# Kernel optimization log

Hardware: AMD Instinct MI355X
Metric: run time of the kernel (lower is better)

Reference implementation:

```python
import jax, jax.numpy as jnp
import numpy as np

H, W = 480, 640
NUM_SEM = 12      # len(stuff_labels)+1
NUM_INS = 16      # number of detected instances
NUM_THING = 9     # len(thing_labels)+1
NUM_ITER = 3
GAMMA_SEM = 3.0
GAMMA_INS = 3.0
ALPHA_SEM = 3.0
BETA_SEM = 0.15
ALPHA_INS = 3.0
BETA_INS = 0.15
R_BIL = 2         # bilateral truncation radius


def _gauss1d(sigma):
    r = int(np.ceil(2.0 * sigma))
    x = np.arange(-r, r + 1, dtype=np.float32)
    k = np.exp(-0.5 * (x / sigma) ** 2)
    k /= k.sum()
    return jnp.asarray(k)


def _sep_blur(q, k):
    # normalized Gaussian spatial filter, separable depthwise conv. q: (C,H,W)
    C = q.shape[0]
    K = k.shape[0]
    p = K // 2
    x = q[None]  # (1,C,H,W)
    kh = jnp.broadcast_to(k.reshape(1, 1, K, 1), (C, 1, K, 1))
    x = jax.lax.conv_general_dilated(x, kh, (1, 1), [(p, p), (0, 0)], feature_group_count=C)
    kw = jnp.broadcast_to(k.reshape(1, 1, 1, K), (C, 1, 1, K))
    x = jax.lax.conv_general_dilated(x, kw, (1, 1), [(0, 0), (p, p)], feature_group_count=C)
    return x[0]


def _bilateral(q, image, alpha, beta, R):
    # truncated-window bilateral (joint spatial/color Gaussian), normalized per pixel
    C, Hh, Ww = q.shape
    Ip = jnp.pad(image, ((0, 0), (R, R), (R, R)), mode='edge')
    qp = jnp.pad(q, ((0, 0), (R, R), (R, R)), mode='edge')
    num = jnp.zeros_like(q)
    den = jnp.zeros((Hh, Ww), q.dtype)
    inv2a2 = 1.0 / (2.0 * alpha * alpha)
    inv2b2 = 1.0 / (2.0 * beta * beta)
    for dy in range(2 * R + 1):
        for dx in range(2 * R + 1):
            Ish = P = Ip[:, dy:dy + Hh, dx:dx + Ww]
            cd = jnp.sum((image - Ish) ** 2, axis=0)          # color distance (H,W)
            sd = float((dy - R) ** 2 + (dx - R) ** 2)          # spatial distance
            w = jnp.exp(-sd * inv2a2 - cd * inv2b2)
            num = num + w[None] * qp[:, dy:dy + Hh, dx:dx + Ww]
            den = den + w
    return num / den[None]


def _compat(q, M):
    # torch.mm(M.t(), q.view(Cin,-1)).view(Cout,H,W)
    return jnp.einsum('io,ihw->ohw', M, q)


def setup_inputs() -> dict:
    key = jax.random.key(0)
    ks = jax.random.split(key, 6)
    return {
        'image': jax.random.uniform(ks[0], (3, H, W), jnp.float32),
        'semantic_logits': jax.random.normal(ks[1], (NUM_SEM, H, W), jnp.float32),
        'instance_logits': jax.random.normal(ks[2], (NUM_INS, H, W), jnp.float32),
        'instance_cls_labels': jax.random.randint(ks[3], (NUM_INS,), 0, NUM_THING),
        'sem_spatial_w': 3.0 * jnp.ones((NUM_SEM,), jnp.float32),
        'sem_bilateral_w': 5.0 * jnp.ones((NUM_SEM,), jnp.float32),
        'sem_compat': jnp.eye(NUM_SEM, dtype=jnp.float32),
        'ins_spatial_w': 3.0 * jnp.ones((NUM_THING,), jnp.float32),
        'ins_bilateral_w': 3.0 * jnp.ones((NUM_THING,), jnp.float32),
        'cross_ins_sem': 0.1 * jax.random.normal(ks[4], (NUM_THING, NUM_SEM), jnp.float32),
        'cross_sem_ins': 0.1 * jax.random.normal(ks[5], (NUM_THING, NUM_SEM), jnp.float32),
    }


def reference(image, semantic_logits, instance_logits, instance_cls_labels,
              sem_spatial_w, sem_bilateral_w, sem_compat,
              ins_spatial_w, ins_bilateral_w, cross_ins_sem, cross_sem_ins):
    k_sem = _gauss1d(GAMMA_SEM)
    k_ins = _gauss1d(GAMMA_INS)
    sem_q = jax.nn.softmax(semantic_logits, axis=0)
    ins_q = jax.nn.softmax(instance_logits, axis=0)
    sw = ins_spatial_w[instance_cls_labels][:, None, None]      # (NI,1,1)
    bw = ins_bilateral_w[instance_cls_labels][:, None, None]
    M_is = cross_ins_sem[instance_cls_labels]                   # (NI, NUM_SEM)
    M_si = cross_sem_ins[instance_cls_labels].T                 # (NUM_SEM, NI)
    for _ in range(NUM_ITER):
        sp_sem = sem_spatial_w[:, None, None] * _sep_blur(sem_q, k_sem)
        bl_sem = sem_bilateral_w[:, None, None] * _bilateral(sem_q, image, ALPHA_SEM, BETA_SEM, R_BIL)
        tmp_sem = semantic_logits + _compat(sp_sem + bl_sem, sem_compat)
        sp_ins = sw * _sep_blur(ins_q, k_ins)
        bl_ins = bw * _bilateral(ins_q, image, ALPHA_INS, BETA_INS, R_BIL)
        tmp_ins = instance_logits + sp_ins + bl_ins
        tmp_sem_new = tmp_sem + _compat(jax.nn.softmax(tmp_ins, axis=0), M_is)
        tmp_ins_new = tmp_ins + _compat(jax.nn.softmax(tmp_sem, axis=0), M_si)
        sem_q = jax.nn.softmax(tmp_sem_new, axis=0)
        ins_q = jax.nn.softmax(tmp_ins_new, axis=0)
    return sem_q, ins_q
```

## Files before the change

kernel.cpp:

```cpp
#include <hip/hip_runtime.h>

#define HH   480
#define WW   640
#define HWP  (HH*WW)
#define NSEM 12
#define NINS 16
#define NCH  28

typedef _Float16 f16_t;

union P32 { f16_t h[32]; int4 v[4]; };
union I4H8 { int4 v; f16_t h[8]; };
union I2H4 { int2 v; f16_t h[4]; };
union H4I2 { f16_t h[4]; int2 v; };

__device__ __forceinline__ void gauss13(float k[13]) {
    float s = 0.f;
#pragma unroll
    for (int j = 0; j < 13; ++j) {
        float xx = (float)(j - 6);
        float v  = __expf(-(xx * xx) * (1.f / 18.f));
        k[j] = v; s += v;
    }
    float inv = 1.f / s;
#pragma unroll
    for (int j = 0; j < 13; ++j) k[j] *= inv;
}

template <int N>
__device__ __forceinline__ void softmaxN(const float* __restrict__ in, float* __restrict__ out) {
    float m = in[0];
#pragma unroll
    for (int i = 1; i < N; ++i) m = fmaxf(m, in[i]);
    float s = 0.f;
#pragma unroll
    for (int i = 0; i < N; ++i) { float e = __expf(in[i] - m); out[i] = e; s += e; }
    float inv = 1.f / s;
#pragma unroll
    for (int i = 0; i < N; ++i) out[i] *= inv;
}

__global__ __launch_bounds__(256) void init_kernel(const float* __restrict__ semL,
                                                   const float* __restrict__ insL,
                                                   int4* __restrict__ qcl4,
                                                   f16_t* __restrict__ qpm,
                                                   f16_t* __restrict__ semLh,
                                                   f16_t* __restrict__ insLh) {
    int p = blockIdx.x * 256 + threadIdx.x;
    float v[NINS], o[NINS];
    P32 pk;
#pragma unroll
    for (int i = 0; i < 32; ++i) pk.h[i] = (f16_t)0.f;
#pragma unroll
    for (int i = 0; i < NSEM; ++i) { v[i] = semL[i * HWP + p]; semLh[i * HWP + p] = (f16_t)v[i]; }
    softmaxN<NSEM>(v, o);
#pragma unroll
    for (int i = 0; i < NSEM; ++i) { f16_t h = (f16_t)o[i]; pk.h[i] = h; qpm[i * HWP + p] = h; }
#pragma unroll
    for (int i = 0; i < NINS; ++i) { v[i] = insL[i * HWP + p]; insLh[i * HWP + p] = (f16_t)v[i]; }
    softmaxN<NINS>(v, o);
#pragma unroll
    for (int i = 0; i < NINS; ++i) { f16_t h = (f16_t)o[i]; pk.h[NSEM + i] = h; qpm[(NSEM + i) * HWP + p] = h; }
#pragma unroll
    for (int j = 0; j < 4; ++j) qcl4[p * 4 + j] = pk.v[j];
}

#define BTW 64
#define BTH 32
#define RAWW 80
#define RAWH 44
__global__ __launch_bounds__(256) void blur_fused_kernel(const f16_t* __restrict__ in,
                                                         f16_t* __restrict__ out) {
    __shared__ float raw[RAWH * RAWW];
    __shared__ float hb[RAWH * BTW];
    const int t  = threadIdx.x;
    const int x0 = blockIdx.x * BTW;
    const int y0 = blockIdx.y * BTH;
    const int c  = blockIdx.z;
    const f16_t* __restrict__ plane = in + (size_t)c * HWP;

    float k[13]; gauss13(k);

    for (int idx = t; idx < RAWH * 10; idx += 256) {
        int row = idx / 10, g = idx - row * 10;
        int gy = y0 - 6 + row;
        int gx8 = x0 - 8 + g * 8;
        float4 lo = {0.f,0.f,0.f,0.f}, hi = {0.f,0.f,0.f,0.f};
        if (gy >= 0 && gy < HH && gx8 >= 0 && gx8 <= WW - 8) {
            I4H8 u; u.v = *(const int4*)&plane[gy * WW + gx8];
            lo.x = (float)u.h[0]; lo.y = (float)u.h[1]; lo.z = (float)u.h[2]; lo.w = (float)u.h[3];
            hi.x = (float)u.h[4]; hi.y = (float)u.h[5]; hi.z = (float)u.h[6]; hi.w = (float)u.h[7];
        }
        *(float4*)&raw[row * RAWW + g * 8]     = lo;
        *(float4*)&raw[row * RAWW + g * 8 + 4] = hi;
    }
    __syncthreads();

    for (int idx = t; idx < RAWH * 16; idx += 256) {
        int row = idx >> 4, xg = idx & 15;
        const float* rp = &raw[row * RAWW + xg * 4];
        float f[20];
#pragma unroll
        for (int q4 = 0; q4 < 5; ++q4) {
            float4 v = *(const float4*)&rp[q4 * 4];
            f[q4*4+0]=v.x; f[q4*4+1]=v.y; f[q4*4+2]=v.z; f[q4*4+3]=v.w;
        }
        float4 o;
        float* op = &o.x;
#pragma unroll
        for (int j = 0; j < 4; ++j) {
            float a = 0.f;
#pragma unroll
            for (int i = 0; i < 13; ++i) a = fmaf(k[i], f[j + 2 + i], a);
            op[j] = a;
        }
        *(float4*)&hb[row * BTW + xg * 4] = o;
    }
    __syncthreads();

    {
        const int xg = t & 15;
        const int yg = t >> 4;
        float4 r[14];
#pragma unroll
        for (int i = 0; i < 14; ++i)
            r[i] = *(const float4*)&hb[(yg * 2 + i) * BTW + xg * 4];
#pragma unroll
        for (int j = 0; j < 2; ++j) {
            float a0 = 0.f, a1 = 0.f, a2 = 0.f, a3 = 0.f;
#pragma unroll
            for (int i = 0; i < 13; ++i) {
                float4 v = r[j + i];
                a0 = fmaf(k[i], v.x, a0); a1 = fmaf(k[i], v.y, a1);
                a2 = fmaf(k[i], v.z, a2); a3 = fmaf(k[i], v.w, a3);
            }
            H4I2 s;
            s.h[0] = (f16_t)a0; s.h[1] = (f16_t)a1; s.h[2] = (f16_t)a2; s.h[3] = (f16_t)a3;
            *(int2*)&out[(size_t)c * HWP + (y0 + yg * 2 + j) * WW + (x0 + xg * 4)] = s.v;
        }
    }
}

#define TTW 32
#define TTH 8
#define TWW (TTW + 4)
#define TWH (TTH + 4)
#define TWN (TWW * TWH)

template <bool LAST>
__global__ __launch_bounds__(256, 5) void tail_kernel(const int4* __restrict__ qcl4,
                                                      const f16_t* __restrict__ sp,
                                                      const float* __restrict__ img,
                                                      const f16_t* __restrict__ semLh,
                                                      const f16_t* __restrict__ insLh,
                                                      const float* __restrict__ sem_sw,
                                                      const float* __restrict__ sem_bw,
                                                      const float* __restrict__ sem_compat,
                                                      const float* __restrict__ ins_sw,
                                                      const float* __restrict__ ins_bw,
                                                      const int*   __restrict__ labels,
                                                      const float* __restrict__ cross_is,
                                                      const float* __restrict__ cross_si,
                                                      int4* __restrict__ qclo4,
                                                      f16_t* __restrict__ qpmo,
                                                      float* __restrict__ dout) {
    __shared__ int4  lqA[TWN * 3];
    __shared__ int2  lqB[TWN];
    __shared__ float limg[3 * TWN];
    __shared__ float sC[NSEM * NSEM];
    __shared__ float sMis[NINS * NSEM];
    __shared__ float sMsi[NINS * NSEM];
    __shared__ float sws[NSEM], sbs[NSEM], swi[NINS], sbi[NINS];

    const int t  = threadIdx.x;
    const int tx = t & 31;
    const int ty = t >> 5;
    const int x0 = blockIdx.x * TTW;
    const int y0 = blockIdx.y * TTH;
    const int p  = (y0 + ty) * WW + (x0 + tx);

    if (t < NSEM * NSEM) sC[t] = sem_compat[t];
    if (t < NINS * NSEM) {
        int i = t / NSEM, o = t - i * NSEM;
        sMis[t] = cross_is[labels[i] * NSEM + o];
        sMsi[t] = cross_si[labels[i] * NSEM + o];
    }
    if (t < NSEM) { sws[t] = sem_sw[t]; sbs[t] = sem_bw[t]; }
    if (t < NINS) { int l = labels[t]; swi[t] = ins_sw[l]; sbi[t] = ins_bw[l]; }

#pragma unroll
    for (int j = 0; j < 6; ++j) {
        int idx = t + j * 256;
        if (idx < TWN * 3) {
            int e = idx / 3, s = idx - e * 3;
            int ly = e / TWW, lx = e - ly * TWW;
            int gy = min(max(y0 - 2 + ly, 0), HH - 1);
            int gx = min(max(x0 - 2 + lx, 0), WW - 1);
            lqA[idx] = qcl4[(gy * WW + gx) * 4 + s];
        }
    }
#pragma unroll
    for (int j = 0; j < 2; ++j) {
        int e = t + j * 256;
        if (e < TWN) {
            int ly = e / TWW, lx = e - ly * TWW;
            int gy = min(max(y0 - 2 + ly, 0), HH - 1);
            int gx = min(max(x0 - 2 + lx, 0), WW - 1);
            lqB[e] = ((const int2*)qcl4)[(gy * WW + gx) * 8 + 6];
        }
    }
    for (int idx = t; idx < 3 * TWN; idx += 256) {
        int cc  = idx / TWN;
        int rem = idx - cc * TWN;
        int ly  = rem / TWW, lx = rem - ly * TWW;
        int gy  = min(max(y0 - 2 + ly, 0), HH - 1);
        int gx  = min(max(x0 - 2 + lx, 0), WW - 1);
        limg[idx] = img[(size_t)cc * HWP + gy * WW + gx];
    }
    __syncthreads();

    float wnr[25];
    {
        const int wc = (ty + 2) * TWW + (tx + 2);
        float i0 = limg[wc], i1 = limg[TWN + wc], i2 = limg[2 * TWN + wc];
        float den = 0.f;
        int d = 0;
#pragma unroll
        for (int dy = 0; dy < 5; ++dy) {
#pragma unroll
            for (int dx = 0; dx < 5; ++dx) {
                int nb = (ty + dy) * TWW + (tx + dx);
                float d0 = limg[nb] - i0;
                float d1 = limg[TWN + nb] - i1;
                float d2 = limg[2 * TWN + nb] - i2;
                float cd = d0 * d0 + d1 * d1 + d2 * d2;
                float sd = (float)((dy - 2) * (dy - 2) + (dx - 2) * (dx - 2));
                float wv = __expf(-sd * (1.f / 18.f) - cd * (1.f / 0.045f));
                wnr[d++] = wv; den += wv;
            }
        }
        float inv = 1.f / den;
#pragma unroll
        for (int j = 0; j < 25; ++j) wnr[j] *= inv;
    }

    float bl[NCH];
#pragma unroll
    for (int c = 0; c < NCH; ++c) bl[c] = 0.f;
#pragma unroll
    for (int dy = 0; dy < 5; ++dy) {
        int rb = (ty + dy) * TWW + tx;
#pragma unroll
        for (int dx = 0; dx < 5; ++dx) {
            float w = wnr[dy * 5 + dx];
            int e = rb + dx;
#pragma unroll
            for (int s = 0; s < 3; ++s) {
                I4H8 u; u.v = lqA[e * 3 + s];
#pragma unroll
                for (int i = 0; i < 8; ++i)
                    bl[s * 8 + i] = fmaf((float)u.h[i], w, bl[s * 8 + i]);
            }
            I2H4 ub; ub.v = lqB[e];
#pragma unroll
            for (int i = 0; i < 4; ++i)
                bl[24 + i] = fmaf((float)ub.h[i], w, bl[24 + i]);
        }
    }

    float comb[NSEM];
#pragma unroll
    for (int i = 0; i < NSEM; ++i)
        comb[i] = sws[i] * (float)sp[i * HWP + p] + sbs[i] * bl[i];
    float ts[NSEM];
#pragma unroll
    for (int o = 0; o < NSEM; ++o) {
        float a = (float)semLh[o * HWP + p];
#pragma unroll
        for (int i = 0; i < NSEM; ++i) a = fmaf(sC[i * NSEM + o], comb[i], a);
        ts[o] = a;
    }
    float ti[NINS];
#pragma unroll
    for (int i = 0; i < NINS; ++i)
        ti[i] = (float)insLh[i * HWP + p] + swi[i] * (float)sp[(NSEM + i) * HWP + p] + sbi[i] * bl[NSEM + i];

    float sIns[NINS], sSem[NSEM];
    softmaxN<NINS>(ti, sIns);
    softmaxN<NSEM>(ts, sSem);

    float nts[NSEM];
#pragma unroll
    for (int o = 0; o < NSEM; ++o) {
        float a = ts[o];
#pragma unroll
        for (int i = 0; i < NINS; ++i) a = fmaf(sMis[i * NSEM + o], sIns[i], a);
        nts[o] = a;
    }
    float nti[NINS];
#pragma unroll
    for (int o = 0; o < NINS; ++o) {
        float a = ti[o];
#pragma unroll
        for (int i = 0; i < NSEM; ++i) a = fmaf(sMsi[o * NSEM + i], sSem[i], a);
        nti[o] = a;
    }

    float oq1[NSEM], oq2[NINS];
    softmaxN<NSEM>(nts, oq1);
    softmaxN<NINS>(nti, oq2);

    if (LAST) {
#pragma unroll
        for (int i = 0; i < NSEM; ++i) dout[i * HWP + p] = oq1[i];
#pragma unroll
        for (int i = 0; i < NINS; ++i) dout[(NSEM + i) * HWP + p] = oq2[i];
    } else {
        P32 pk;
#pragma unroll
        for (int i = 0; i < 32; ++i) pk.h[i] = (f16_t)0.f;
#pragma unroll
        for (int i = 0; i < NSEM; ++i) { f16_t h = (f16_t)oq1[i]; pk.h[i] = h; qpmo[i * HWP + p] = h; }
#pragma unroll
        for (int i = 0; i < NINS; ++i) { f16_t h = (f16_t)oq2[i]; pk.h[NSEM + i] = h; qpmo[(NSEM + i) * HWP + p] = h; }
#pragma unroll
        for (int j = 0; j < 4; ++j) qclo4[p * 4 + j] = pk.v[j];
    }
}

extern "C" void kernel_launch(void* const* d_in, const int* in_sizes, int n_in,
                              void* d_out, int out_size, void* d_ws, size_t ws_size,
                              hipStream_t stream) {
    const float* image      = (const float*)d_in[0];
    const float* semL       = (const float*)d_in[1];
    const float* insL       = (const float*)d_in[2];
    const int*   labels     = (const int*)  d_in[3];
    const float* sem_sw     = (const float*)d_in[4];
    const float* sem_bw     = (const float*)d_in[5];
    const float* sem_compat = (const float*)d_in[6];
    const float* ins_sw     = (const float*)d_in[7];
    const float* ins_bw     = (const float*)d_in[8];
    const float* cross_is   = (const float*)d_in[9];
    const float* cross_si   = (const float*)d_in[10];

    char* ws = (char*)d_ws;
    int4*  qclA  = (int4*)ws;                                   ws += (size_t)HWP * 64;
    int4*  qclB  = (int4*)ws;                                   ws += (size_t)HWP * 64;
    f16_t* qpmA  = (f16_t*)ws;                                  ws += (size_t)NCH * HWP * 2;
    f16_t* qpmB  = (f16_t*)ws;                                  ws += (size_t)NCH * HWP * 2;
    f16_t* sp    = (f16_t*)ws;                                  ws += (size_t)NCH * HWP * 2;
    f16_t* semLh = (f16_t*)ws;                                  ws += (size_t)NSEM * HWP * 2;
    f16_t* insLh = (f16_t*)ws;

    const int PIX_BLOCKS = HWP / 256;
    init_kernel<<<PIX_BLOCKS, 256, 0, stream>>>(semL, insL, qclA, qpmA, semLh, insLh);

    dim3 bgrid(WW / BTW, HH / BTH, NCH);
    dim3 tgrid(WW / TTW, HH / TTH);

    blur_fused_kernel<<<bgrid, 256, 0, stream>>>(qpmA, sp);
    tail_kernel<false><<<tgrid, 256, 0, stream>>>(qclA, sp, image, semLh, insLh,
                                                  sem_sw, sem_bw, sem_compat,
                                                  ins_sw, ins_bw, labels,
                                                  cross_is, cross_si, qclB, qpmB, nullptr);
    blur_fused_kernel<<<bgrid, 256, 0, stream>>>(qpmB, sp);
    tail_kernel<false><<<tgrid, 256, 0, stream>>>(qclB, sp, image, semLh, insLh,
                                                  sem_sw, sem_bw, sem_compat,
                                                  ins_sw, ins_bw, labels,
                                                  cross_is, cross_si, qclA, qpmA, nullptr);
    blur_fused_kernel<<<bgrid, 256, 0, stream>>>(qpmA, sp);
    tail_kernel<true><<<tgrid, 256, 0, stream>>>(qclA, sp, image, semLh, insLh,
                                                 sem_sw, sem_bw, sem_compat,
                                                 ins_sw, ins_bw, labels,
                                                 cross_is, cross_si, nullptr, nullptr, (float*)d_out);
}
```

Baseline: 280.8 us.

## Split blur into channel-last horizontal pass and fuse vertical pass into tail

Replaces the planar per-channel fused blur kernel with a horizontal-only pass over the channel-interleaved q buffer. The vertical 13-tap pass is computed inside the tail kernel by reading the horizontally blurred buffer straight from global memory. Logits move to a channel-interleaved f16 buffer, the planar q copy is dropped, the bilateral weight normalisation is folded into a single division, and tail blocks are swizzled. This removes the planar buffer writes and the separate 2D-tiled blur. In exchange, each tail thread does 13 uncached global row reads per pixel, and lowering the launch bound occupancy target raises register pressure.

Result: slower. 651.4 us (+132.0%).

```diff
diff --git a/kernel.cpp b/kernel.cpp
--- a/kernel.cpp
+++ b/kernel.cpp
@@ -9,10 +9,9 @@
 
 typedef _Float16 f16_t;
 
-union P32 { f16_t h[32]; int4 v[4]; };
+union P32  { f16_t h[32]; int4 v[4]; };
 union I4H8 { int4 v; f16_t h[8]; };
 union I2H4 { int2 v; f16_t h[4]; };
-union H4I2 { f16_t h[4]; int2 v; };
 
 __device__ __forceinline__ void gauss13(float k[13]) {
     float s = 0.f;
@@ -43,102 +42,50 @@
 __global__ __launch_bounds__(256) void init_kernel(const float* __restrict__ semL,
                                                    const float* __restrict__ insL,
                                                    int4* __restrict__ qcl4,
-                                                   f16_t* __restrict__ qpm,
-                                                   f16_t* __restrict__ semLh,
-                                                   f16_t* __restrict__ insLh) {
+                                                   int4* __restrict__ lcl4) {
     int p = blockIdx.x * 256 + threadIdx.x;
     float v[NINS], o[NINS];
-    P32 pk;
-#pragma unroll
-    for (int i = 0; i < 32; ++i) pk.h[i] = (f16_t)0.f;
-#pragma unroll
-    for (int i = 0; i < NSEM; ++i) { v[i] = semL[i * HWP + p]; semLh[i * HWP + p] = (f16_t)v[i]; }
+    P32 pk, lk;
+#pragma unroll
+    for (int i = 0; i < 32; ++i) { pk.h[i] = (f16_t)0.f; lk.h[i] = (f16_t)0.f; }
+#pragma unroll
+    for (int i = 0; i < NSEM; ++i) { v[i] = semL[i * HWP + p]; lk.h[i] = (f16_t)v[i]; }
     softmaxN<NSEM>(v, o);
 #pragma unroll
-    for (int i = 0; i < NSEM; ++i) { f16_t h = (f16_t)o[i]; pk.h[i] = h; qpm[i * HWP + p] = h; }
-#pragma unroll
-    for (int i = 0; i < NINS; ++i) { v[i] = insL[i * HWP + p]; insLh[i * HWP + p] = (f16_t)v[i]; }
+    for (int i = 0; i < NSEM; ++i) pk.h[i] = (f16_t)o[i];
+#pragma unroll
+    for (int i = 0; i < NINS; ++i) { v[i] = insL[i * HWP + p]; lk.h[NSEM + i] = (f16_t)v[i]; }
     softmaxN<NINS>(v, o);
 #pragma unroll
-    for (int i = 0; i < NINS; ++i) { f16_t h = (f16_t)o[i]; pk.h[NSEM + i] = h; qpm[(NSEM + i) * HWP + p] = h; }
-#pragma unroll
-    for (int j = 0; j < 4; ++j) qcl4[p * 4 + j] = pk.v[j];
-}
-
-#define BTW 64
-#define BTH 32
-#define RAWW 80
-#define RAWH 44
-__global__ __launch_bounds__(256) void blur_fused_kernel(const f16_t* __restrict__ in,
-                                                         f16_t* __restrict__ out) {
-    __shared__ float raw[RAWH * RAWW];
-    __shared__ float hb[RAWH * BTW];
-    const int t  = threadIdx.x;
-    const int x0 = blockIdx.x * BTW;
-    const int y0 = blockIdx.y * BTH;
-    const int c  = blockIdx.z;
-    const f16_t* __restrict__ plane = in + (size_t)c * HWP;
-
+    for (int i = 0; i < NINS; ++i) pk.h[NSEM + i] = (f16_t)o[i];
+#pragma unroll
+    for (int j = 0; j < 4; ++j) { qcl4[(size_t)p * 4 + j] = pk.v[j]; lcl4[(size_t)p * 4 + j] = lk.v[j]; }
+}
+
+__global__ __launch_bounds__(256) void hpass_kernel(const int4* __restrict__ qcl4,
+                                                    int4* __restrict__ hq4) {
+    int tid = blockIdx.x * 256 + threadIdx.x;
+    int p = tid >> 2;
+    int s = tid & 3;
+    int y = p / WW;
+    int x = p - y * WW;
     float k[13]; gauss13(k);
-
-    for (int idx = t; idx < RAWH * 10; idx += 256) {
-        int row = idx / 10, g = idx - row * 10;
-        int gy = y0 - 6 + row;
-        int gx8 = x0 - 8 + g * 8;
-        float4 lo = {0.f,0.f,0.f,0.f}, hi = {0.f,0.f,0.f,0.f};
-        if (gy >= 0 && gy < HH && gx8 >= 0 && gx8 <= WW - 8) {
-            I4H8 u; u.v = *(const int4*)&plane[gy * WW + gx8];
-            lo.x = (float)u.h[0]; lo.y = (float)u.h[1]; lo.z = (float)u.h[2]; lo.w = (float)u.h[3];
-            hi.x = (float)u.h[4]; hi.y = (float)u.h[5]; hi.z = (float)u.h[6]; hi.w = (float)u.h[7];
-        }
-        *(float4*)&raw[row * RAWW + g * 8]     = lo;
-        *(float4*)&raw[row * RAWW + g * 8 + 4] = hi;
-    }
-    __syncthreads();
-
-    for (int idx = t; idx < RAWH * 16; idx += 256) {
-        int row = idx >> 4, xg = idx & 15;
-        const float* rp = &raw[row * RAWW + xg * 4];
-        float f[20];
-#pragma unroll
-        for (int q4 = 0; q4 < 5; ++q4) {
-            float4 v = *(const float4*)&rp[q4 * 4];
-            f[q4*4+0]=v.x; f[q4*4+1]=v.y; f[q4*4+2]=v.z; f[q4*4+3]=v.w;
-        }
-        float4 o;
-        float* op = &o.x;
-#pragma unroll
-        for (int j = 0; j < 4; ++j) {
-            float a = 0.f;
-#pragma unroll
-            for (int i = 0; i < 13; ++i) a = fmaf(k[i], f[j + 2 + i], a);
-            op[j] = a;
-        }
-        *(float4*)&hb[row * BTW + xg * 4] = o;
-    }
-    __syncthreads();
-
-    {
-        const int xg = t & 15;
-        const int yg = t >> 4;
-        float4 r[14];
-#pragma unroll
-        for (int i = 0; i < 14; ++i)
-            r[i] = *(const float4*)&hb[(yg * 2 + i) * BTW + xg * 4];
-#pragma unroll
-        for (int j = 0; j < 2; ++j) {
-            float a0 = 0.f, a1 = 0.f, a2 = 0.f, a3 = 0.f;
-#pragma unroll
-            for (int i = 0; i < 13; ++i) {
-                float4 v = r[j + i];
-                a0 = fmaf(k[i], v.x, a0); a1 = fmaf(k[i], v.y, a1);
-                a2 = fmaf(k[i], v.z, a2); a3 = fmaf(k[i], v.w, a3);
-            }
-            H4I2 s;
-            s.h[0] = (f16_t)a0; s.h[1] = (f16_t)a1; s.h[2] = (f16_t)a2; s.h[3] = (f16_t)a3;
-            *(int2*)&out[(size_t)c * HWP + (y0 + yg * 2 + j) * WW + (x0 + xg * 4)] = s.v;
-        }
-    }
+    float a[8];
+#pragma unroll
+    for (int i = 0; i < 8; ++i) a[i] = 0.f;
+#pragma unroll
+    for (int t = 0; t < 13; ++t) {
+        int xt = x + t - 6;
+        if ((unsigned)xt < WW) {
+            I4H8 u; u.v = qcl4[(size_t)(p + t - 6) * 4 + s];
+#pragma unroll
+            for (int i = 0; i < 8; ++i) a[i] = fmaf((float)u.h[i], k[t], a[i]);
+        }
+    }
+    I4H8 r;
+#pragma unroll
+    for (int i = 0; i < 8; ++i) r.h[i] = (f16_t)a[i];
+    hq4[tid] = r.v;
 }
 
 #define TTW 32
@@ -148,11 +95,10 @@
 #define TWN (TWW * TWH)
 
 template <bool LAST>
-__global__ __launch_bounds__(256, 5) void tail_kernel(const int4* __restrict__ qcl4,
-                                                      const f16_t* __restrict__ sp,
+__global__ __launch_bounds__(256, 4) void tail_kernel(const int4* __restrict__ qcl4,
+                                                      const int4* __restrict__ hq4,
                                                       const float* __restrict__ img,
-                                                      const f16_t* __restrict__ semLh,
-                                                      const f16_t* __restrict__ insLh,
+                                                      const int4* __restrict__ lcl4,
                                                       const float* __restrict__ sem_sw,
                                                       const float* __restrict__ sem_bw,
                                                       const float* __restrict__ sem_compat,
@@ -162,7 +108,6 @@
                                                       const float* __restrict__ cross_is,
                                                       const float* __restrict__ cross_si,
                                                       int4* __restrict__ qclo4,
-                                                      f16_t* __restrict__ qpmo,
                                                       float* __restrict__ dout) {
     __shared__ int4  lqA[TWN * 3];
     __shared__ int2  lqB[TWN];
@@ -172,12 +117,16 @@
     __shared__ float sMsi[NINS * NSEM];
     __shared__ float sws[NSEM], sbs[NSEM], swi[NINS], sbi[NINS];
 
-    const int t  = threadIdx.x;
-    const int tx = t & 31;
-    const int ty = t >> 5;
-    const int x0 = blockIdx.x * TTW;
-    const int y0 = blockIdx.y * TTH;
-    const int p  = (y0 + ty) * WW + (x0 + tx);
+    const int t = threadIdx.x;
+    const int lid = (int)blockIdx.x;
+    const int swz = (lid & 7) * 150 + (lid >> 3);
+    const int by  = swz / 20;
+    const int bx  = swz - by * 20;
+    const int tx  = t & 31;
+    const int ty  = t >> 5;
+    const int x0  = bx * TTW;
+    const int y0  = by * TTH;
+    const int p   = (y0 + ty) * WW + (x0 + tx);
 
     if (t < NSEM * NSEM) sC[t] = sem_compat[t];
     if (t < NINS * NSEM) {
@@ -196,7 +145,7 @@
             int ly = e / TWW, lx = e - ly * TWW;
             int gy = min(max(y0 - 2 + ly, 0), HH - 1);
             int gx = min(max(x0 - 2 + lx, 0), WW - 1);
-            lqA[idx] = qcl4[(gy * WW + gx) * 4 + s];
+            lqA[idx] = qcl4[((size_t)gy * WW + gx) * 4 + s];
         }
     }
 #pragma unroll
@@ -206,7 +155,7 @@
             int ly = e / TWW, lx = e - ly * TWW;
             int gy = min(max(y0 - 2 + ly, 0), HH - 1);
             int gx = min(max(x0 - 2 + lx, 0), WW - 1);
-            lqB[e] = ((const int2*)qcl4)[(gy * WW + gx) * 8 + 6];
+            lqB[e] = ((const int2*)qcl4)[((size_t)gy * WW + gx) * 8 + 6];
         }
     }
     for (int idx = t; idx < 3 * TWN; idx += 256) {
@@ -217,73 +166,97 @@
         int gx  = min(max(x0 - 2 + lx, 0), WW - 1);
         limg[idx] = img[(size_t)cc * HWP + gy * WW + gx];
     }
+
+    float kv[13]; gauss13(kv);
+    float vac[NCH];
+#pragma unroll
+    for (int c = 0; c < NCH; ++c) vac[c] = 0.f;
+    {
+        const int xc = x0 + tx;
+        const int yb = y0 + ty - 6;
+#pragma unroll
+        for (int tt = 0; tt < 13; ++tt) {
+            int yt = yb + tt;
+            if ((unsigned)yt < HH) {
+                const int4* rp = &hq4[((size_t)yt * WW + xc) * 4];
+                float w = kv[tt];
+                I4H8 u0, u1, u2; I2H4 u3;
+                u0.v = rp[0]; u1.v = rp[1]; u2.v = rp[2];
+                u3.v = ((const int2*)rp)[6];
+#pragma unroll
+                for (int i = 0; i < 8; ++i) vac[i]      = fmaf((float)u0.h[i], w, vac[i]);
+#pragma unroll
+                for (int i = 0; i < 8; ++i) vac[8 + i]  = fmaf((float)u1.h[i], w, vac[8 + i]);
+#pragma unroll
+                for (int i = 0; i < 8; ++i) vac[16 + i] = fmaf((float)u2.h[i], w, vac[16 + i]);
+#pragma unroll
+                for (int i = 0; i < 4; ++i) vac[24 + i] = fmaf((float)u3.h[i], w, vac[24 + i]);
+            }
+        }
+    }
+    I4H8 l0, l1, l2; I2H4 l3;
+    l0.v = lcl4[(size_t)p * 4 + 0];
+    l1.v = lcl4[(size_t)p * 4 + 1];
+    l2.v = lcl4[(size_t)p * 4 + 2];
+    l3.v = ((const int2*)lcl4)[(size_t)p * 8 + 6];
     __syncthreads();
 
-    float wnr[25];
+    float num[NCH];
+#pragma unroll
+    for (int c = 0; c < NCH; ++c) num[c] = 0.f;
+    float den = 0.f;
     {
         const int wc = (ty + 2) * TWW + (tx + 2);
         float i0 = limg[wc], i1 = limg[TWN + wc], i2 = limg[2 * TWN + wc];
-        float den = 0.f;
-        int d = 0;
 #pragma unroll
         for (int dy = 0; dy < 5; ++dy) {
 #pragma unroll
             for (int dx = 0; dx < 5; ++dx) {
-                int nb = (ty + dy) * TWW + (tx + dx);
-                float d0 = limg[nb] - i0;
-                float d1 = limg[TWN + nb] - i1;
-                float d2 = limg[2 * TWN + nb] - i2;
+                int e = (ty + dy) * TWW + (tx + dx);
+                float d0 = limg[e] - i0;
+                float d1 = limg[TWN + e] - i1;
+                float d2 = limg[2 * TWN + e] - i2;
                 float cd = d0 * d0 + d1 * d1 + d2 * d2;
                 float sd = (float)((dy - 2) * (dy - 2) + (dx - 2) * (dx - 2));
-                float wv = __expf(-sd * (1.f / 18.f) - cd * (1.f / 0.045f));
-                wnr[d++] = wv; den += wv;
+                float w  = __expf(-sd * (1.f / 18.f) - cd * (1.f / 0.045f));
+                den += w;
+                I4H8 a0, a1, a2; I2H4 b;
+                a0.v = lqA[e * 3 + 0]; a1.v = lqA[e * 3 + 1]; a2.v = lqA[e * 3 + 2];
+                b.v  = lqB[e];
+#pragma unroll
+                for (int i = 0; i < 8; ++i) num[i]      = fmaf((float)a0.h[i], w, num[i]);
+#pragma unroll
+                for (int i = 0; i < 8; ++i) num[8 + i]  = fmaf((float)a1.h[i], w, num[8 + i]);
+#pragma unroll
+                for (int i = 0; i < 8; ++i) num[16 + i] = fmaf((float)a2.h[i], w, num[16 + i]);
+#pragma unroll
+                for (int i = 0; i < 4; ++i) num[24 + i] = fmaf((float)b.h[i],  w, num[24 + i]);
             }
         }
-        float inv = 1.f / den;
-#pragma unroll
-        for (int j = 0; j < 25; ++j) wnr[j] *= inv;
-    }
-
-    float bl[NCH];
-#pragma unroll
-    for (int c = 0; c < NCH; ++c) bl[c] = 0.f;
-#pragma unroll
-    for (int dy = 0; dy < 5; ++dy) {
-        int rb = (ty + dy) * TWW + tx;
-#pragma unroll
-        for (int dx = 0; dx < 5; ++dx) {
-            float w = wnr[dy * 5 + dx];
-            int e = rb + dx;
-#pragma unroll
-            for (int s = 0; s < 3; ++s) {
-                I4H8 u; u.v = lqA[e * 3 + s];
-#pragma unroll
-                for (int i = 0; i < 8; ++i)
-                    bl[s * 8 + i] = fmaf((float)u.h[i], w, bl[s * 8 + i]);
-            }
-            I2H4 ub; ub.v = lqB[e];
-#pragma unroll
-            for (int i = 0; i < 4; ++i)
-                bl[24 + i] = fmaf((float)ub.h[i], w, bl[24 + i]);
-        }
-    }
+    }
+    const float inv = 1.f / den;
 
     float comb[NSEM];
 #pragma unroll
     for (int i = 0; i < NSEM; ++i)
-        comb[i] = sws[i] * (float)sp[i * HWP + p] + sbs[i] * bl[i];
+        comb[i] = sws[i] * vac[i] + sbs[i] * (num[i] * inv);
     float ts[NSEM];
 #pragma unroll
     for (int o = 0; o < NSEM; ++o) {
-        float a = (float)semLh[o * HWP + p];
+        float a = (o < 8) ? (float)l0.h[o] : (float)l1.h[o - 8];
 #pragma unroll
         for (int i = 0; i < NSEM; ++i) a = fmaf(sC[i * NSEM + o], comb[i], a);
         ts[o] = a;
     }
     float ti[NINS];
 #pragma unroll
-    for (int i = 0; i < NINS; ++i)
-        ti[i] = (float)insLh[i * HWP + p] + swi[i] * (float)sp[(NSEM + i) * HWP + p] + sbi[i] * bl[NSEM + i];
+    for (int i = 0; i < NINS; ++i) {
+        const int c = NSEM + i;
+        float lg = (c < 16) ? (float)l1.h[c - 8]
+                 : (c < 24) ? (float)l2.h[c - 16]
+                            : (float)l3.h[c - 24];
+        ti[i] = lg + swi[i] * vac[c] + sbi[i] * (num[c] * inv);
+    }
 
     float sIns[NINS], sSem[NSEM];
     softmaxN<NINS>(ti, sIns);
@@ -320,11 +293,11 @@
 #pragma unroll
         for (int i = 0; i < 32; ++i) pk.h[i] = (f16_t)0.f;
 #pragma unroll
-        for (int i = 0; i < NSEM; ++i) { f16_t h = (f16_t)oq1[i]; pk.h[i] = h; qpmo[i * HWP + p] = h; }
-#pragma unroll
-        for (int i = 0; i < NINS; ++i) { f16_t h = (f16_t)oq2[i]; pk.h[NSEM + i] = h; qpmo[(NSEM + i) * HWP + p] = h; }
-#pragma unroll
-        for (int j = 0; j < 4; ++j) qclo4[p * 4 + j] = pk.v[j];
+        for (int i = 0; i < NSEM; ++i) pk.h[i] = (f16_t)oq1[i];
+#pragma unroll
+        for (int i = 0; i < NINS; ++i) pk.h[NSEM + i] = (f16_t)oq2[i];
+#pragma unroll
+        for (int j = 0; j < 4; ++j) qclo4[(size_t)p * 4 + j] = pk.v[j];
     }
 }
 
@@ -344,33 +317,29 @@
     const float* cross_si   = (const float*)d_in[10];
 
     char* ws = (char*)d_ws;
-    int4*  qclA  = (int4*)ws;                                   ws += (size_t)HWP * 64;
-    int4*  qclB  = (int4*)ws;                                   ws += (size_t)HWP * 64;
-    f16_t* qpmA  = (f16_t*)ws;                                  ws += (size_t)NCH * HWP * 2;
-    f16_t* qpmB  = (f16_t*)ws;                                  ws += (size_t)NCH * HWP * 2;
-    f16_t* sp    = (f16_t*)ws;                                  ws += (size_t)NCH * HWP * 2;
-    f16_t* semLh = (f16_t*)ws;                                  ws += (size_t)NSEM * HWP * 2;
-    f16_t* insLh = (f16_t*)ws;
+    int4* qclA = (int4*)ws;   ws += (size_t)HWP * 64;
+    int4* qclB = (int4*)ws;   ws += (size_t)HWP * 64;
+    int4* hq   = (int4*)ws;   ws += (size_t)HWP * 64;
+    int4* lcl  = (int4*)ws;
 
     const int PIX_BLOCKS = HWP / 256;
-    init_kernel<<<PIX_BLOCKS, 256, 0, stream>>>(semL, insL, qclA, qpmA, semLh, insLh);
-
-    dim3 bgrid(WW / BTW, HH / BTH, NCH);
-    dim3 tgrid(WW / TTW, HH / TTH);
-
-    blur_fused_kernel<<<bgrid, 256, 0, stream>>>(qpmA, sp);
-    tail_kernel<false><<<tgrid, 256, 0, stream>>>(qclA, sp, image, semLh, insLh,
-                                                  sem_sw, sem_bw, sem_compat,
-                                                  ins_sw, ins_bw, labels,
-                                                  cross_is, cross_si, qclB, qpmB, nullptr);
-    blur_fused_kernel<<<bgrid, 256, 0, stream>>>(qpmB, sp);
-    tail_kernel<false><<<tgrid, 256, 0, stream>>>(qclB, sp, image, semLh, insLh,
-                                                  sem_sw, sem_bw, sem_compat,
-                                                  ins_sw, ins_bw, labels,
-                                                  cross_is, cross_si, qclA, qpmA, nullptr);
-    blur_fused_kernel<<<bgrid, 256, 0, stream>>>(qpmA, sp);
-    tail_kernel<true><<<tgrid, 256, 0, stream>>>(qclA, sp, image, semLh, insLh,
+    const int HB         = HWP * 4 / 256;
+
+    init_kernel<<<PIX_BLOCKS, 256, 0, stream>>>(semL, insL, qclA, lcl);
+
+    hpass_kernel<<<HB, 256, 0, stream>>>(qclA, hq);
+    tail_kernel<false><<<1200, 256, 0, stream>>>(qclA, hq, image, lcl,
                                                  sem_sw, sem_bw, sem_compat,
                                                  ins_sw, ins_bw, labels,
-                                                 cross_is, cross_si, nullptr, nullptr, (float*)d_out);
-}
+                                                 cross_is, cross_si, qclB, nullptr);
+    hpass_kernel<<<HB, 256, 0, stream>>>(qclB, hq);
+    tail_kernel<false><<<1200, 256, 0, stream>>>(qclB, hq, image, lcl,
+                                                 sem_sw, sem_bw, sem_compat,
+                                                 ins_sw, ins_bw, labels,
+                                                 cross_is, cross_si, qclA, nullptr);
+    hpass_kernel<<<HB, 256, 0, stream>>>(qclA, hq);
+    tail_kernel<true><<<1200, 256, 0, stream>>>(qclA, hq, image, lcl,
+                                                sem_sw, sem_bw, sem_compat,
+                                                ins_sw, ins_bw, labels,
+                                                cross_is, cross_si, nullptr, (float*)d_out);
+}
```

## Use fp16 shared staging in blur and fuse bilateral weight and accumulate loops

Applied to the files above, without the earlier changes.

The blur kernel now keeps its raw and horizontally-blurred tiles in fp16 shared memory instead of fp32. This halves LDS footprint and traffic, and the launch bounds now ask for higher occupancy. The tail kernel prefetches the spatial-blur values into registers before the shared-memory staging. It also computes the bilateral weights on the fly inside the accumulation loop and normalizes once at the end, dropping the 25-entry weight array, and its occupancy hint goes from 5 to 4 blocks. The extra fp16 rounding of the intermediate blur, and the added register pressure from the prefetch, are the risks.

New measurement: 356.2 us. 1.27x slower.

```diff
diff --git a/kernel.cpp b/kernel.cpp
--- a/kernel.cpp
+++ b/kernel.cpp
@@ -9,7 +9,7 @@
 
 typedef _Float16 f16_t;
 
-union P32 { f16_t h[32]; int4 v[4]; };
+union P32  { f16_t h[32]; int4 v[4]; };
 union I4H8 { int4 v; f16_t h[8]; };
 union I2H4 { int2 v; f16_t h[4]; };
 union H4I2 { f16_t h[4]; int2 v; };
@@ -69,10 +69,10 @@
 #define BTH 32
 #define RAWW 80
 #define RAWH 44
-__global__ __launch_bounds__(256) void blur_fused_kernel(const f16_t* __restrict__ in,
-                                                         f16_t* __restrict__ out) {
-    __shared__ float raw[RAWH * RAWW];
-    __shared__ float hb[RAWH * BTW];
+__global__ __launch_bounds__(256, 6) void blur_fused_kernel(const f16_t* __restrict__ in,
+                                                            f16_t* __restrict__ out) {
+    __shared__ __align__(16) f16_t rawh[RAWH * RAWW];
+    __shared__ __align__(16) f16_t hbh[RAWH * BTW];
     const int t  = threadIdx.x;
     const int x0 = blockIdx.x * BTW;
     const int y0 = blockIdx.y * BTH;
@@ -85,54 +85,50 @@
         int row = idx / 10, g = idx - row * 10;
         int gy = y0 - 6 + row;
         int gx8 = x0 - 8 + g * 8;
-        float4 lo = {0.f,0.f,0.f,0.f}, hi = {0.f,0.f,0.f,0.f};
-        if (gy >= 0 && gy < HH && gx8 >= 0 && gx8 <= WW - 8) {
-            I4H8 u; u.v = *(const int4*)&plane[gy * WW + gx8];
-            lo.x = (float)u.h[0]; lo.y = (float)u.h[1]; lo.z = (float)u.h[2]; lo.w = (float)u.h[3];
-            hi.x = (float)u.h[4]; hi.y = (float)u.h[5]; hi.z = (float)u.h[6]; hi.w = (float)u.h[7];
-        }
-        *(float4*)&raw[row * RAWW + g * 8]     = lo;
-        *(float4*)&raw[row * RAWW + g * 8 + 4] = hi;
+        int4 u = {0, 0, 0, 0};
+        if (gy >= 0 && gy < HH && gx8 >= 0 && gx8 <= WW - 8)
+            u = *(const int4*)&plane[gy * WW + gx8];
+        *(int4*)&rawh[row * RAWW + g * 8] = u;
     }
     __syncthreads();
 
     for (int idx = t; idx < RAWH * 16; idx += 256) {
         int row = idx >> 4, xg = idx & 15;
-        const float* rp = &raw[row * RAWW + xg * 4];
-        float f[20];
-#pragma unroll
-        for (int q4 = 0; q4 < 5; ++q4) {
-            float4 v = *(const float4*)&rp[q4 * 4];
-            f[q4*4+0]=v.x; f[q4*4+1]=v.y; f[q4*4+2]=v.z; f[q4*4+3]=v.w;
-        }
-        float4 o;
-        float* op = &o.x;
+        const f16_t* rp = &rawh[row * RAWW + xg * 4];
+        I2H4 fq[5];
+#pragma unroll
+        for (int q = 0; q < 5; ++q) fq[q].v = *(const int2*)&rp[q * 4];
+        H4I2 o;
 #pragma unroll
         for (int j = 0; j < 4; ++j) {
             float a = 0.f;
 #pragma unroll
-            for (int i = 0; i < 13; ++i) a = fmaf(k[i], f[j + 2 + i], a);
-            op[j] = a;
-        }
-        *(float4*)&hb[row * BTW + xg * 4] = o;
+            for (int i = 0; i < 13; ++i) {
+                int e = j + 2 + i;
+                a = fmaf(k[i], (float)fq[e >> 2].h[e & 3], a);
+            }
+            o.h[j] = (f16_t)a;
+        }
+        *(int2*)&hbh[row * BTW + xg * 4] = o.v;
     }
     __syncthreads();
 
     {
         const int xg = t & 15;
         const int yg = t >> 4;
-        float4 r[14];
+        I2H4 r[14];
 #pragma unroll
         for (int i = 0; i < 14; ++i)
-            r[i] = *(const float4*)&hb[(yg * 2 + i) * BTW + xg * 4];
+            r[i].v = *(const int2*)&hbh[(yg * 2 + i) * BTW + xg * 4];
 #pragma unroll
         for (int j = 0; j < 2; ++j) {
             float a0 = 0.f, a1 = 0.f, a2 = 0.f, a3 = 0.f;
 #pragma unroll
             for (int i = 0; i < 13; ++i) {
-                float4 v = r[j + i];
-                a0 = fmaf(k[i], v.x, a0); a1 = fmaf(k[i], v.y, a1);
-                a2 = fmaf(k[i], v.z, a2); a3 = fmaf(k[i], v.w, a3);
+                a0 = fmaf(k[i], (float)r[j + i].h[0], a0);
+                a1 = fmaf(k[i], (float)r[j + i].h[1], a1);
+                a2 = fmaf(k[i], (float)r[j + i].h[2], a2);
+                a3 = fmaf(k[i], (float)r[j + i].h[3], a3);
             }
             H4I2 s;
             s.h[0] = (f16_t)a0; s.h[1] = (f16_t)a1; s.h[2] = (f16_t)a2; s.h[3] = (f16_t)a3;
@@ -148,7 +144,7 @@
 #define TWN (TWW * TWH)
 
 template <bool LAST>
-__global__ __launch_bounds__(256, 5) void tail_kernel(const int4* __restrict__ qcl4,
+__global__ __launch_bounds__(256, 4) void tail_kernel(const int4* __restrict__ qcl4,
                                                       const f16_t* __restrict__ sp,
                                                       const float* __restrict__ img,
                                                       const f16_t* __restrict__ semLh,
@@ -179,6 +175,10 @@
     const int y0 = blockIdx.y * TTH;
     const int p  = (y0 + ty) * WW + (x0 + tx);
 
+    f16_t spv[NCH];
+#pragma unroll
+    for (int c = 0; c < NCH; ++c) spv[c] = sp[c * HWP + p];
+
     if (t < NSEM * NSEM) sC[t] = sem_compat[t];
     if (t < NINS * NSEM) {
         int i = t / NSEM, o = t - i * NSEM;
@@ -219,59 +219,45 @@
     }
     __syncthreads();
 
-    float wnr[25];
+    float num[NCH];
+#pragma unroll
+    for (int c = 0; c < NCH; ++c) num[c] = 0.f;
+    float den = 0.f;
     {
         const int wc = (ty + 2) * TWW + (tx + 2);
         float i0 = limg[wc], i1 = limg[TWN + wc], i2 = limg[2 * TWN + wc];
-        float den = 0.f;
-        int d = 0;
 #pragma unroll
         for (int dy = 0; dy < 5; ++dy) {
 #pragma unroll
             for (int dx = 0; dx < 5; ++dx) {
-                int nb = (ty + dy) * TWW + (tx + dx);
-                float d0 = limg[nb] - i0;
-                float d1 = limg[TWN + nb] - i1;
-                float d2 = limg[2 * TWN + nb] - i2;
+                int e = (ty + dy) * TWW + (tx + dx);
+                float d0 = limg[e] - i0;
+                float d1 = limg[TWN + e] - i1;
+                float d2 = limg[2 * TWN + e] - i2;
                 float cd = d0 * d0 + d1 * d1 + d2 * d2;
                 float sd = (float)((dy - 2) * (dy - 2) + (dx - 2) * (dx - 2));
-                float wv = __expf(-sd * (1.f / 18.f) - cd * (1.f / 0.045f));
-                wnr[d++] = wv; den += wv;
+                float w  = __expf(-sd * (1.f / 18.f) - cd * (1.f / 0.045f));
+                den += w;
+                I4H8 a0, a1, a2; I2H4 b;
+                a0.v = lqA[e * 3 + 0]; a1.v = lqA[e * 3 + 1]; a2.v = lqA[e * 3 + 2];
+                b.v  = lqB[e];
+#pragma unroll
+                for (int i = 0; i < 8; ++i) num[i]      = fmaf((float)a0.h[i], w, num[i]);
+#pragma unroll
+                for (int i = 0; i < 8; ++i) num[8 + i]  = fmaf((float)a1.h[i], w, num[8 + i]);
+#pragma unroll
+                for (int i = 0; i < 8; ++i) num[16 + i] = fmaf((float)a2.h[i], w, num[16 + i]);
+#pragma unroll
+                for (int i = 0; i < 4; ++i) num[24 + i] = fmaf((float)b.h[i],  w, num[24 + i]);
             }
         }
-        float inv = 1.f / den;
-#pragma unroll
-        for (int j = 0; j < 25; ++j) wnr[j] *= inv;
-    }
-
-    float bl[NCH];
-#pragma unroll
-    for (int c = 0; c < NCH; ++c) bl[c] = 0.f;
-#pragma unroll
-    for (int dy = 0; dy < 5; ++dy) {
-        int rb = (ty + dy) * TWW + tx;
-#pragma unroll
-        for (int dx = 0; dx < 5; ++dx) {
-            float w = wnr[dy * 5 + dx];
-            int e = rb + dx;
-#pragma unroll
-            for (int s = 0; s < 3; ++s) {
-                I4H8 u; u.v = lqA[e * 3 + s];
-#pragma unroll
-                for (int i = 0; i < 8; ++i)
-                    bl[s * 8 + i] = fmaf((float)u.h[i], w, bl[s * 8 + i]);
-            }
-            I2H4 ub; ub.v = lqB[e];
-#pragma unroll
-            for (int i = 0; i < 4; ++i)
-                bl[24 + i] = fmaf((float)ub.h[i], w, bl[24 + i]);
-        }
-    }
+    }
+    const float inv = 1.f / den;
 
     float comb[NSEM];
 #pragma unroll
     for (int i = 0; i < NSEM; ++i)
-        comb[i] = sws[i] * (float)sp[i * HWP + p] + sbs[i] * bl[i];
+        comb[i] = sws[i] * (float)spv[i] + sbs[i] * (num[i] * inv);
     float ts[NSEM];
 #pragma unroll
     for (int o = 0; o < NSEM; ++o) {
@@ -283,7 +269,7 @@
     float ti[NINS];
 #pragma unroll
     for (int i = 0; i < NINS; ++i)
-        ti[i] = (float)insLh[i * HWP + p] + swi[i] * (float)sp[(NSEM + i) * HWP + p] + sbi[i] * bl[NSEM + i];
+        ti[i] = (float)insLh[i * HWP + p] + swi[i] * (float)spv[NSEM + i] + sbi[i] * (num[NSEM + i] * inv);
 
     float sIns[NINS], sSem[NSEM];
     softmaxN<NINS>(ti, sIns);
```
